# Kernel optimization log

Hardware: AMD Instinct MI355X
Metric: run time of the kernel (lower is better)

## Reference

```python
import jax, jax.numpy as jnp
import numpy as np

SP = 4      # sp_size (number of simulated sequence-parallel ranks)
NH = 16     # num_attention_heads
HD = 64     # head_dim
HS = 1024   # hidden_size
B = 1       # batch
S = 8192    # global sequence length (SP chunks of 2048)


def setup_inputs() -> dict:
    key = jax.random.key(0)
    ks = jax.random.split(key, 9)
    w_scale = 1.0 / np.sqrt(HS)
    def w(k):
        # xavier-ish init, stored as [in, out] so y = x @ W + b
        return jax.random.uniform(k, (HS, HS), jnp.float32, -w_scale, w_scale)
    return {
        'hidden_states': jax.random.normal(ks[0], (B, S, HS), jnp.float32),
        'Wq': w(ks[1]), 'bq': jnp.zeros((HS,), jnp.float32),
        'Wk': w(ks[2]), 'bk': jnp.zeros((HS,), jnp.float32),
        'Wv': w(ks[3]), 'bv': jnp.zeros((HS,), jnp.float32),
        'Wo': w(ks[4]), 'bo': jnp.zeros((HS,), jnp.float32),
    }


def reference(hidden_states, Wq, bq, Wk, bk, Wv, bv, Wo, bo):
    b, s, _ = hidden_states.shape
    sc = s // SP  # per-rank chunk length
    inv_sqrt_hd = 1.0 / np.sqrt(HD)

    def heads(x):
        # [B, S, HS] -> [SP, B, NH, Sc, HD]
        return x.reshape(b, SP, sc, NH, HD).transpose(1, 0, 3, 2, 4)

    q = heads(hidden_states @ Wq + bq)
    k = heads(hidden_states @ Wk + bk)
    v = heads(hidden_states @ Wv + bv)

    out = jnp.zeros_like(q)
    # ring attention: at step i each rank r attends to chunk (r + i) mod SP
    for i in range(SP):
        ki = jnp.roll(k, -i, axis=0)
        vi = jnp.roll(v, -i, axis=0)
        scores = jnp.einsum('sbhqd,sbhkd->sbhqk', q, ki) * inv_sqrt_hd
        probs = jax.nn.softmax(scores, axis=-1)  # per-chunk softmax (faithful to source)
        out = out + jnp.einsum('sbhqk,sbhkd->sbhqd', probs, vi)
    out = out / SP  # source divides accumulated context by sp_size

    # [SP, B, NH, Sc, HD] -> [B, S, NH*HD]
    ctx = out.transpose(1, 0, 3, 2, 4).reshape(b, s, NH * HD)
    return ctx @ Wo + bo
```

## Files before the change

kernel.cpp:

```cpp
#include <hip/hip_runtime.h>

#define DEVINL __device__ __forceinline__

typedef __attribute__((ext_vector_type(8))) short short8;
typedef __attribute__((ext_vector_type(4))) float floatx4;
typedef __attribute__((ext_vector_type(2))) unsigned uintx2;

DEVINL unsigned short f2bf(float f){
  unsigned u = __builtin_bit_cast(unsigned, f);
  u += 0x7FFFu + ((u >> 16) & 1u);
  return (unsigned short)(u >> 16);
}
DEVINL unsigned pk2(float a, float b){
  unsigned ua = __builtin_bit_cast(unsigned, a);
  unsigned ub = __builtin_bit_cast(unsigned, b);
  ua += 0x7FFFu + ((ua >> 16) & 1u);
  ub += 0x7FFFu + ((ub >> 16) & 1u);
  return (ua >> 16) | (ub & 0xFFFF0000u);
}
DEVINL unsigned pkfast(float a, float b){
  unsigned ua = __builtin_bit_cast(unsigned, a) + 0x8000u;
  unsigned ub = __builtin_bit_cast(unsigned, b) + 0x8000u;
  return __builtin_amdgcn_perm(ub, ua, 0x07060302u);
}
DEVINL float bf2f(unsigned short h){
  unsigned u = ((unsigned)h) << 16;
  return __builtin_bit_cast(float, u);
}
DEVINL void gload_lds16(const void* g, void* l){
  __builtin_amdgcn_global_load_lds((const __attribute__((address_space(1))) void*)g,
                                   (__attribute__((address_space(3))) void*)l, 16, 0, 0);
}
DEVINL int perm2(int k){
  return (((k >> 4) & 1) << 5) | (((k >> 2) & 3) << 3) | (((k >> 5) & 1) << 2) | (k & 3);
}

__global__ void k_detect(const unsigned* __restrict__ w, int* __restrict__ flag){
  __shared__ int cnt;
  if (threadIdx.x == 0) cnt = 0;
  __syncthreads();
  int c = 0;
  for (int i = threadIdx.x; i < 1024; i += 256){
    unsigned e = (w[i] >> 7) & 0xFFu;
    c += (e >= 120u && e <= 132u) ? 1 : 0;
  }
  atomicAdd(&cnt, c);
  __syncthreads();
  if (threadIdx.x == 0) *flag = (cnt > 512) ? 1 : 0;
}

__global__ void k_conv_bf16(const void* __restrict__ src, unsigned short* __restrict__ dst,
                            int n, const int* __restrict__ flag){
  int i = (blockIdx.x * 256 + threadIdx.x) * 8;
  if (i >= n) return;
  if (*flag){
    ((uint4*)dst)[i >> 3] = ((const uint4*)src)[i >> 3];
  } else {
    const float* s = (const float*)src;
    short8 v;
    #pragma unroll
    for (int j = 0; j < 8; j++) v[j] = (short)f2bf(s[i + j]);
    *(short8*)(dst + i) = v;
  }
}

__global__ void k_conv_wT4(const void* __restrict__ s0, const void* __restrict__ s1,
                           const void* __restrict__ s2, const void* __restrict__ s3,
                           unsigned short* __restrict__ d0, unsigned short* __restrict__ d1,
                           unsigned short* __restrict__ d2, unsigned short* __restrict__ d3,
                           const int* __restrict__ flag){
  __shared__ float tile[32][33];
  const void* src; unsigned short* dst;
  switch (blockIdx.z){
    case 0: src = s0; dst = d0; break;
    case 1: src = s1; dst = d1; break;
    case 2: src = s2; dst = d2; break;
    default: src = s3; dst = d3; break;
  }
  const int tx = threadIdx.x & 31, ty = threadIdx.x >> 5;
  const int bx = blockIdx.x, by = blockIdx.y;
  const int isbf = *flag;
  #pragma unroll
  for (int r = 0; r < 32; r += 8){
    int k = by*32 + ty + r, n = bx*32 + tx;
    float v = isbf ? bf2f(((const unsigned short*)src)[k*1024 + n])
                   : ((const float*)src)[k*1024 + n];
    tile[ty + r][tx] = v;
  }
  __syncthreads();
  #pragma unroll
  for (int r = 0; r < 32; r += 8){
    int n = bx*32 + ty + r, k = by*32 + tx;
    dst[n*1024 + k] = f2bf(tile[tx][ty + r]);
  }
}

__global__ void k_conv_b4(const void* __restrict__ s0, const void* __restrict__ s1,
                          const void* __restrict__ s2, const void* __restrict__ s3,
                          float* __restrict__ dst, const int* __restrict__ flag){
  int i = blockIdx.x * 256 + threadIdx.x;
  if (i >= 4096) return;
  int z = i >> 10, j = i & 1023;
  const void* s = (z == 0) ? s0 : (z == 1) ? s1 : (z == 2) ? s2 : s3;
  dst[i] = (*flag) ? bf2f(((const unsigned short*)s)[j]) : ((const float*)s)[j];
}

template<int MODE>
__global__ __launch_bounds__(256, 2) void k_gemm(
    const unsigned short* __restrict__ A, const unsigned short* __restrict__ Bt,
    const float* __restrict__ bias, void* __restrict__ C0, void* __restrict__ C1,
    void* __restrict__ C2, const int* __restrict__ flagp, float scale)
{
  const int K = 1024;
  __shared__ __align__(16) unsigned short As[128*32];
  __shared__ __align__(16) unsigned short Bs[128*32];
  const int tid = threadIdx.x;
  const int lane = tid & 63, wave = tid >> 6;
  const int quad = lane >> 4, l15 = lane & 15;
  const int m0 = blockIdx.x * 128, n0 = blockIdx.y * 128;
  const int wm = (wave >> 1) * 64, wn = (wave & 1) * 64;
  const floatx4 fzero = {0.f, 0.f, 0.f, 0.f};
  floatx4 acc[4][4];
  #pragma unroll
  for (int i = 0; i < 4; i++)
    #pragma unroll
    for (int j = 0; j < 4; j++) acc[i][j] = fzero;

  for (int k0 = 0; k0 < K; k0 += 32){
    __syncthreads();
    #pragma unroll
    for (int rep = 0; rep < 2; rep++){
      int idx = tid + rep*256;
      int row = idx >> 2, c = idx & 3;
      gload_lds16(A  + (size_t)(m0 + row)*K + (k0 + c*8), &As[idx*8]);
      gload_lds16(Bt + (size_t)(n0 + row)*K + (k0 + c*8), &Bs[idx*8]);
    }
    asm volatile("s_waitcnt vmcnt(0)" ::: "memory");
    __syncthreads();
    short8 af[4], bf[4];
    #pragma unroll
    for (int i = 0; i < 4; i++) af[i] = *(const short8*)&As[(wm + i*16 + l15)*32 + quad*8];
    #pragma unroll
    for (int j = 0; j < 4; j++) bf[j] = *(const short8*)&Bs[(wn + j*16 + l15)*32 + quad*8];
    #pragma unroll
    for (int i = 0; i < 4; i++)
      #pragma unroll
      for (int j = 0; j < 4; j++)
        acc[i][j] = __builtin_amdgcn_mfma_f32_16x16x32_bf16(af[i], bf[j], acc[i][j], 0, 0, 0);
  }

  float bs[4];
  #pragma unroll
  for (int j = 0; j < 4; j++) bs[j] = bias[n0 + wn + j*16 + l15];
  const int useBf = (MODE == 1) ? *flagp : 1;
  #pragma unroll
  for (int i = 0; i < 4; i++){
    #pragma unroll
    for (int j = 0; j < 4; j++){
      int n = n0 + wn + j*16 + l15;
      #pragma unroll
      for (int r = 0; r < 4; r++){
        int m = m0 + wm + i*16 + quad*4 + r;
        float v = acc[i][j][r] + bs[j];
        if (MODE == 3){
          int sel = n >> 10, nn = n & 1023;
          if (sel == 0){
            int dd = (nn & 63) ^ ((m & 7) << 3);
            ((unsigned short*)C0)[((size_t)(nn >> 6)*8192 + m)*64 + dd] = f2bf(v * scale);
          } else if (sel == 1){
            int dd = (nn & 63) ^ ((m & 7) << 3);
            ((unsigned short*)C1)[((size_t)(nn >> 6)*8192 + m)*64 + dd] = f2bf(v);
          } else {
            int s2 = perm2(m & 63) ^ ((nn & 7) << 3);
            ((unsigned short*)C2)[(size_t)nn*8192 + (m & ~63) + s2] = f2bf(v);
          }
        } else {
          if (useBf) ((unsigned short*)C0)[(size_t)m*1024 + n] = f2bf(v);
          else       ((float*)C0)[(size_t)m*1024 + n] = v;
        }
      }
    }
  }
}

__global__ __launch_bounds__(256, 2) void k_attn(
    const unsigned short* __restrict__ Qg, const unsigned short* __restrict__ Kg,
    const unsigned short* __restrict__ Vg, unsigned short* __restrict__ ctx)
{
  __shared__ __align__(16) unsigned short Qs[256*64];
  __shared__ __align__(16) unsigned short Ks[2][64*64];
  __shared__ __align__(16) unsigned short Vs[2][64*64];
  const int tid = threadIdx.x, lane = tid & 63, wave = tid >> 6;
  const int quad = lane >> 4, l15 = lane & 15;
  const int bid = blockIdx.x;
  const int xcd = bid & 7, slot = bid >> 3;
  const int h = xcd*2 + (slot >> 5);
  const int rem = slot & 31, rchunk = rem >> 3, qt = rem & 7;
  const int sq0 = rchunk*2048 + qt*256;
  const char* Qbase = (const char*)(Qg + (size_t)h*8192*64 + (size_t)sq0*64);
  const char* Kbase = (const char*)(Kg + (size_t)h*8192*64);
  const char* Vbase = (const char*)(Vg + (size_t)h*8192*64);
  const int wq0 = wave * 64;
  const floatx4 fzero = {0.f, 0.f, 0.f, 0.f};

  const int idx0 = tid, idx1 = tid + 256;
  const size_t voff0 = (size_t)(idx0 >> 3)*16384 + (idx0 & 7)*16;
  const size_t voff1 = (size_t)(idx1 >> 3)*16384 + (idx1 & 7)*16;

  auto stage = [&](int buf, int kvs){
    const char* Kt = Kbase + (size_t)kvs*128;
    const char* Vt = Vbase + (size_t)kvs*2;
    char* kd = (char*)Ks[buf];
    char* vd = (char*)Vs[buf];
    gload_lds16(Kt + idx0*16, kd + idx0*16);
    gload_lds16(Kt + idx1*16, kd + idx1*16);
    gload_lds16(Vt + voff0, vd + idx0*16);
    gload_lds16(Vt + voff1, vd + idx1*16);
  };

  #pragma unroll
  for (int rep = 0; rep < 8; rep++){
    int idx = tid + rep*256;
    gload_lds16(Qbase + idx*16, (char*)Qs + idx*16);
  }
  stage(0, rchunk*2048);
  asm volatile("s_waitcnt vmcnt(0)" ::: "memory");
  __syncthreads();

  short8 qf[4][2];
  #pragma unroll
  for (int mi = 0; mi < 4; mi++)
    #pragma unroll
    for (int ks = 0; ks < 2; ks++){
      int row = wq0 + mi*16 + l15;
      qf[mi][ks] = *(const short8*)&Qs[row*64 + (((ks*4 + quad) ^ (row & 7)))*8];
    }

  short8 ones;
  #pragma unroll
  for (int j = 0; j < 8; j++) ones[j] = (short)0x3F80;

  floatx4 Of[4][4];
  #pragma unroll
  for (int mi = 0; mi < 4; mi++)
    #pragma unroll
    for (int di = 0; di < 4; di++) Of[mi][di] = fzero;

  for (int i = 0; i < 4; i++){
    floatx4 Oc[4][4], Ol[4];
    #pragma unroll
    for (int mi = 0; mi < 4; mi++){
      Ol[mi] = fzero;
      #pragma unroll
      for (int di = 0; di < 4; di++) Oc[mi][di] = fzero;
    }

    for (int kt = 0; kt < 32; kt++){
      const int t = i*32 + kt, cur = t & 1;
      asm volatile("s_waitcnt vmcnt(0)" ::: "memory");
      __syncthreads();
      if (t < 127){
        int t1 = t + 1;
        int kvs = ((rchunk + (t1 >> 5)) & 3)*2048 + (t1 & 31)*64;
        stage(cur ^ 1, kvs);
      }

      short8 pf[4][2];
      #pragma unroll
      for (int mi = 0; mi < 4; mi++){
        floatx4 St[4];
        #pragma unroll
        for (int ni = 0; ni < 4; ni++) St[ni] = fzero;
        #pragma unroll
        for (int ks = 0; ks < 2; ks++)
          #pragma unroll
          for (int ni = 0; ni < 4; ni++){
            int krow = ni*16 + l15;
            short8 kf = *(const short8*)&Ks[cur][krow*64 + (((ks*4 + quad) ^ (krow & 7)))*8];
            St[ni] = __builtin_amdgcn_mfma_f32_16x16x32_bf16(kf, qf[mi][ks], St[ni], 0, 0, 0);
          }
        #pragma unroll
        for (int ni = 0; ni < 4; ni++)
          #pragma unroll
          for (int r = 0; r < 4; r++)
            St[ni][r] = __builtin_amdgcn_exp2f(St[ni][r]);
        #pragma unroll
        for (int ks = 0; ks < 2; ks++){
          uintx2 lo, hi;
          lo[0] = pkfast(St[ks  ][0], St[ks  ][1]);
          lo[1] = pkfast(St[ks  ][2], St[ks  ][3]);
          hi[0] = pkfast(St[2+ks][0], St[2+ks][1]);
          hi[1] = pkfast(St[2+ks][2], St[2+ks][3]);
          union { uintx2 u[2]; short8 s; } cv;
          cv.u[0] = lo; cv.u[1] = hi;
          pf[mi][ks] = cv.s;
        }
      }

      #pragma unroll
      for (int ks = 0; ks < 2; ks++){
        #pragma unroll
        for (int di = 0; di < 4; di++){
          int vrow = di*16 + l15;
          short8 vf = *(const short8*)&Vs[cur][vrow*64 + (((ks*4 + quad) ^ (vrow & 7)))*8];
          #pragma unroll
          for (int mi = 0; mi < 4; mi++)
            Oc[mi][di] = __builtin_amdgcn_mfma_f32_16x16x32_bf16(vf, pf[mi][ks], Oc[mi][di], 0, 0, 0);
        }
        #pragma unroll
        for (int mi = 0; mi < 4; mi++)
          Ol[mi] = __builtin_amdgcn_mfma_f32_16x16x32_bf16(ones, pf[mi][ks], Ol[mi], 0, 0, 0);
      }
    }

    #pragma unroll
    for (int mi = 0; mi < 4; mi++){
      float inv = __builtin_amdgcn_rcpf(Ol[mi][0]);
      #pragma unroll
      for (int di = 0; di < 4; di++)
        #pragma unroll
        for (int r = 0; r < 4; r++) Of[mi][di][r] += Oc[mi][di][r] * inv;
    }
  }

  #pragma unroll
  for (int mi = 0; mi < 4; mi++){
    int q = sq0 + wq0 + mi*16 + l15;
    #pragma unroll
    for (int di = 0; di < 4; di++){
      uintx2 w;
      w[0] = pk2(Of[mi][di][0]*0.25f, Of[mi][di][1]*0.25f);
      w[1] = pk2(Of[mi][di][2]*0.25f, Of[mi][di][3]*0.25f);
      *(uintx2*)&ctx[(size_t)q*1024 + h*64 + di*16 + quad*4] = w;
    }
  }
}

extern "C" void kernel_launch(void* const* d_in, const int* in_sizes, int n_in,
                              void* d_out, int out_size, void* d_ws, size_t ws_size,
                              hipStream_t stream)
{
  (void)in_sizes; (void)n_in; (void)out_size; (void)ws_size;
  char* ws = (char*)d_ws;
  size_t off = 0;
  auto alloc = [&](size_t bytes) -> char* {
    char* p = ws + off;
    off = (off + bytes + 255) & ~(size_t)255;
    return p;
  };
  int* flag            = (int*)alloc(4);
  unsigned short* hsb  = (unsigned short*)alloc((size_t)8192*1024*2);
  unsigned short* wqt  = (unsigned short*)alloc((size_t)1024*1024*2);
  unsigned short* wkt  = (unsigned short*)alloc((size_t)1024*1024*2);
  unsigned short* wvt  = (unsigned short*)alloc((size_t)1024*1024*2);
  unsigned short* wot  = (unsigned short*)alloc((size_t)1024*1024*2);
  float* biasAll       = (float*)alloc(4096*4);
  unsigned short* Qb   = (unsigned short*)alloc((size_t)16*8192*64*2);
  unsigned short* Kb   = (unsigned short*)alloc((size_t)16*8192*64*2);
  unsigned short* Vb   = (unsigned short*)alloc((size_t)16*8192*64*2);
  unsigned short* ctxb = (unsigned short*)alloc((size_t)8192*1024*2);

  k_detect<<<1, 256, 0, stream>>>((const unsigned*)d_in[0], flag);
  k_conv_bf16<<<4096, 256, 0, stream>>>(d_in[0], hsb, 8192*1024, flag);
  k_conv_wT4<<<dim3(32,32,4), 256, 0, stream>>>(d_in[1], d_in[3], d_in[5], d_in[7],
                                                wqt, wkt, wvt, wot, flag);
  k_conv_b4<<<16, 256, 0, stream>>>(d_in[2], d_in[4], d_in[6], d_in[8], biasAll, flag);

  const float Cs = 0.18033688011112042f;
  k_gemm<3><<<dim3(64, 24), 256, 0, stream>>>(hsb, wqt, biasAll, Qb, Kb, Vb, nullptr, Cs);

  k_attn<<<512, 256, 0, stream>>>(Qb, Kb, Vb, ctxb);

  k_gemm<1><<<dim3(64, 8), 256, 0, stream>>>(ctxb, wot, biasAll + 3072, d_out,
                                             nullptr, nullptr, flag, 1.0f);
}
```

Baseline: 483.1 us.

## Halve attention query tile to 128 rows, double grid, drop Q LDS staging

```diff
diff --git a/kernel.cpp b/kernel.cpp
--- a/kernel.cpp
+++ b/kernel.cpp
@@ -183,24 +183,23 @@
   }
 }
 
-__global__ __launch_bounds__(256, 2) void k_attn(
+__global__ __launch_bounds__(256, 4) void k_attn(
     const unsigned short* __restrict__ Qg, const unsigned short* __restrict__ Kg,
     const unsigned short* __restrict__ Vg, unsigned short* __restrict__ ctx)
 {
-  __shared__ __align__(16) unsigned short Qs[256*64];
   __shared__ __align__(16) unsigned short Ks[2][64*64];
   __shared__ __align__(16) unsigned short Vs[2][64*64];
   const int tid = threadIdx.x, lane = tid & 63, wave = tid >> 6;
   const int quad = lane >> 4, l15 = lane & 15;
   const int bid = blockIdx.x;
   const int xcd = bid & 7, slot = bid >> 3;
-  const int h = xcd*2 + (slot >> 5);
-  const int rem = slot & 31, rchunk = rem >> 3, qt = rem & 7;
-  const int sq0 = rchunk*2048 + qt*256;
-  const char* Qbase = (const char*)(Qg + (size_t)h*8192*64 + (size_t)sq0*64);
+  const int h = xcd*2 + (slot >> 6);
+  const int rem = slot & 63, rchunk = rem >> 4, qt = rem & 15;
+  const int sq0 = rchunk*2048 + qt*128;
+  const unsigned short* Qp = Qg + (size_t)h*8192*64 + (size_t)sq0*64;
   const char* Kbase = (const char*)(Kg + (size_t)h*8192*64);
   const char* Vbase = (const char*)(Vg + (size_t)h*8192*64);
-  const int wq0 = wave * 64;
+  const int wq0 = wave * 32;
   const floatx4 fzero = {0.f, 0.f, 0.f, 0.f};
 
   const int idx0 = tid, idx1 = tid + 256;
@@ -218,38 +217,33 @@
     gload_lds16(Vt + voff1, vd + idx1*16);
   };
 
-  #pragma unroll
-  for (int rep = 0; rep < 8; rep++){
-    int idx = tid + rep*256;
-    gload_lds16(Qbase + idx*16, (char*)Qs + idx*16);
-  }
+  short8 qf[2][2];
+  #pragma unroll
+  for (int mi = 0; mi < 2; mi++)
+    #pragma unroll
+    for (int ks = 0; ks < 2; ks++){
+      int row = wq0 + mi*16 + l15;
+      qf[mi][ks] = *(const short8*)&Qp[row*64 + (((ks*4 + quad) ^ (row & 7)))*8];
+    }
+
   stage(0, rchunk*2048);
   asm volatile("s_waitcnt vmcnt(0)" ::: "memory");
   __syncthreads();
 
-  short8 qf[4][2];
-  #pragma unroll
-  for (int mi = 0; mi < 4; mi++)
-    #pragma unroll
-    for (int ks = 0; ks < 2; ks++){
-      int row = wq0 + mi*16 + l15;
-      qf[mi][ks] = *(const short8*)&Qs[row*64 + (((ks*4 + quad) ^ (row & 7)))*8];
-    }
-
   short8 ones;
   #pragma unroll
   for (int j = 0; j < 8; j++) ones[j] = (short)0x3F80;
 
-  floatx4 Of[4][4];
-  #pragma unroll
-  for (int mi = 0; mi < 4; mi++)
+  floatx4 Of[2][4];
+  #pragma unroll
+  for (int mi = 0; mi < 2; mi++)
     #pragma unroll
     for (int di = 0; di < 4; di++) Of[mi][di] = fzero;
 
   for (int i = 0; i < 4; i++){
-    floatx4 Oc[4][4], Ol[4];
-    #pragma unroll
-    for (int mi = 0; mi < 4; mi++){
+    floatx4 Oc[2][4], Ol[2];
+    #pragma unroll
+    for (int mi = 0; mi < 2; mi++){
       Ol[mi] = fzero;
       #pragma unroll
       for (int di = 0; di < 4; di++) Oc[mi][di] = fzero;
@@ -265,35 +259,38 @@
         stage(cur ^ 1, kvs);
       }
 
-      short8 pf[4][2];
-      #pragma unroll
-      for (int mi = 0; mi < 4; mi++){
-        floatx4 St[4];
-        #pragma unroll
-        for (int ni = 0; ni < 4; ni++) St[ni] = fzero;
-        #pragma unroll
-        for (int ks = 0; ks < 2; ks++)
+      short8 pf[2][2];
+      #pragma unroll
+      for (int g = 0; g < 2; g++){
+        floatx4 Sa[2], Sb[2];
+        #pragma unroll
+        for (int mi = 0; mi < 2; mi++){ Sa[mi] = fzero; Sb[mi] = fzero; }
+        #pragma unroll
+        for (int ks = 0; ks < 2; ks++){
+          int krowA = g*16 + l15, krowB = (g + 2)*16 + l15;
+          short8 kfa = *(const short8*)&Ks[cur][krowA*64 + (((ks*4 + quad) ^ (krowA & 7)))*8];
+          short8 kfb = *(const short8*)&Ks[cur][krowB*64 + (((ks*4 + quad) ^ (krowB & 7)))*8];
           #pragma unroll
-          for (int ni = 0; ni < 4; ni++){
-            int krow = ni*16 + l15;
-            short8 kf = *(const short8*)&Ks[cur][krow*64 + (((ks*4 + quad) ^ (krow & 7)))*8];
-            St[ni] = __builtin_amdgcn_mfma_f32_16x16x32_bf16(kf, qf[mi][ks], St[ni], 0, 0, 0);
+          for (int mi = 0; mi < 2; mi++){
+            Sa[mi] = __builtin_amdgcn_mfma_f32_16x16x32_bf16(kfa, qf[mi][ks], Sa[mi], 0, 0, 0);
+            Sb[mi] = __builtin_amdgcn_mfma_f32_16x16x32_bf16(kfb, qf[mi][ks], Sb[mi], 0, 0, 0);
           }
-        #pragma unroll
-        for (int ni = 0; ni < 4; ni++)
+        }
+        #pragma unroll
+        for (int mi = 0; mi < 2; mi++){
           #pragma unroll
-          for (int r = 0; r < 4; r++)
-            St[ni][r] = __builtin_amdgcn_exp2f(St[ni][r]);
-        #pragma unroll
-        for (int ks = 0; ks < 2; ks++){
+          for (int r = 0; r < 4; r++){
+            Sa[mi][r] = __builtin_amdgcn_exp2f(Sa[mi][r]);
+            Sb[mi][r] = __builtin_amdgcn_exp2f(Sb[mi][r]);
+          }
           uintx2 lo, hi;
-          lo[0] = pkfast(St[ks  ][0], St[ks  ][1]);
-          lo[1] = pkfast(St[ks  ][2], St[ks  ][3]);
-          hi[0] = pkfast(St[2+ks][0], St[2+ks][1]);
-          hi[1] = pkfast(St[2+ks][2], St[2+ks][3]);
+          lo[0] = pkfast(Sa[mi][0], Sa[mi][1]);
+          lo[1] = pkfast(Sa[mi][2], Sa[mi][3]);
+          hi[0] = pkfast(Sb[mi][0], Sb[mi][1]);
+          hi[1] = pkfast(Sb[mi][2], Sb[mi][3]);
           union { uintx2 u[2]; short8 s; } cv;
           cv.u[0] = lo; cv.u[1] = hi;
-          pf[mi][ks] = cv.s;
+          pf[mi][g] = cv.s;
         }
       }
 
@@ -303,18 +300,16 @@
         for (int di = 0; di < 4; di++){
           int vrow = di*16 + l15;
           short8 vf = *(const short8*)&Vs[cur][vrow*64 + (((ks*4 + quad) ^ (vrow & 7)))*8];
-          #pragma unroll
-          for (int mi = 0; mi < 4; mi++)
-            Oc[mi][di] = __builtin_amdgcn_mfma_f32_16x16x32_bf16(vf, pf[mi][ks], Oc[mi][di], 0, 0, 0);
+          Oc[0][di] = __builtin_amdgcn_mfma_f32_16x16x32_bf16(vf, pf[0][ks], Oc[0][di], 0, 0, 0);
+          Oc[1][di] = __builtin_amdgcn_mfma_f32_16x16x32_bf16(vf, pf[1][ks], Oc[1][di], 0, 0, 0);
         }
-        #pragma unroll
-        for (int mi = 0; mi < 4; mi++)
-          Ol[mi] = __builtin_amdgcn_mfma_f32_16x16x32_bf16(ones, pf[mi][ks], Ol[mi], 0, 0, 0);
+        Ol[0] = __builtin_amdgcn_mfma_f32_16x16x32_bf16(ones, pf[0][ks], Ol[0], 0, 0, 0);
+        Ol[1] = __builtin_amdgcn_mfma_f32_16x16x32_bf16(ones, pf[1][ks], Ol[1], 0, 0, 0);
       }
     }
 
     #pragma unroll
-    for (int mi = 0; mi < 4; mi++){
+    for (int mi = 0; mi < 2; mi++){
       float inv = __builtin_amdgcn_rcpf(Ol[mi][0]);
       #pragma unroll
       for (int di = 0; di < 4; di++)
@@ -324,7 +319,7 @@
   }
 
   #pragma unroll
-  for (int mi = 0; mi < 4; mi++){
+  for (int mi = 0; mi < 2; mi++){
     int q = sq0 + wq0 + mi*16 + l15;
     #pragma unroll
     for (int di = 0; di < 4; di++){
@@ -369,7 +364,7 @@
   const float Cs = 0.18033688011112042f;
   k_gemm<3><<<dim3(64, 24), 256, 0, stream>>>(hsb, wqt, biasAll, Qb, Kb, Vb, nullptr, Cs);
 
-  k_attn<<<512, 256, 0, stream>>>(Qb, Kb, Vb, ctxb);
+  k_attn<<<1024, 256, 0, stream>>>(Qb, Kb, Vb, ctxb);
 
   k_gemm<1><<<dim3(64, 8), 256, 0, stream>>>(ctxb, wot, biasAll + 3072, d_out,
                                              nullptr, nullptr, flag, 1.0f);
```

New measurement: 507.8 us. 1.05x slower.

## Restructure attention inner loop: VALU row sums, reload Q from LDS, unroll buffers

Applied to the files above, without the earlier changes.

```diff
diff --git a/kernel.cpp b/kernel.cpp
--- a/kernel.cpp
+++ b/kernel.cpp
@@ -188,8 +188,7 @@
     const unsigned short* __restrict__ Vg, unsigned short* __restrict__ ctx)
 {
   __shared__ __align__(16) unsigned short Qs[256*64];
-  __shared__ __align__(16) unsigned short Ks[2][64*64];
-  __shared__ __align__(16) unsigned short Vs[2][64*64];
+  __shared__ __align__(16) unsigned short KV[2*64*64*2];
   const int tid = threadIdx.x, lane = tid & 63, wave = tid >> 6;
   const int quad = lane >> 4, l15 = lane & 15;
   const int bid = blockIdx.x;
@@ -210,8 +209,8 @@
   auto stage = [&](int buf, int kvs){
     const char* Kt = Kbase + (size_t)kvs*128;
     const char* Vt = Vbase + (size_t)kvs*2;
-    char* kd = (char*)Ks[buf];
-    char* vd = (char*)Vs[buf];
+    char* kd = (char*)KV + buf*8192;
+    char* vd = (char*)KV + 16384 + buf*8192;
     gload_lds16(Kt + idx0*16, kd + idx0*16);
     gload_lds16(Kt + idx1*16, kd + idx1*16);
     gload_lds16(Vt + voff0, vd + idx0*16);
@@ -224,104 +223,109 @@
     gload_lds16(Qbase + idx*16, (char*)Qs + idx*16);
   }
   stage(0, rchunk*2048);
+
+  const int swz0 = ((0*4 + quad) ^ (l15 & 7)) * 16;
+  const int swz1 = ((1*4 + quad) ^ (l15 & 7)) * 16;
+  const char* kvb0 = (const char*)KV + l15*128 + swz0;
+  const char* kvb1 = (const char*)KV + l15*128 + swz1;
+  const char* qb0  = (const char*)Qs + (wq0 + l15)*128 + swz0;
+  const char* qb1  = (const char*)Qs + (wq0 + l15)*128 + swz1;
+
   asm volatile("s_waitcnt vmcnt(0)" ::: "memory");
   __syncthreads();
 
-  short8 qf[4][2];
+  floatx4 Of[4][4];
   #pragma unroll
   for (int mi = 0; mi < 4; mi++)
     #pragma unroll
-    for (int ks = 0; ks < 2; ks++){
-      int row = wq0 + mi*16 + l15;
-      qf[mi][ks] = *(const short8*)&Qs[row*64 + (((ks*4 + quad) ^ (row & 7)))*8];
-    }
-
-  short8 ones;
-  #pragma unroll
-  for (int j = 0; j < 8; j++) ones[j] = (short)0x3F80;
-
-  floatx4 Of[4][4];
-  #pragma unroll
-  for (int mi = 0; mi < 4; mi++)
-    #pragma unroll
     for (int di = 0; di < 4; di++) Of[mi][di] = fzero;
 
+#define TILE_BODY(CUR, TT)                                                          \
+  {                                                                                 \
+    asm volatile("s_waitcnt vmcnt(0)" ::: "memory");            \
+    __syncthreads();                                         \
+    if ((TT) < 127){                                                                \
+      int t1 = (TT) + 1;                                                            \
+      int kvs = ((rchunk + (t1 >> 5)) & 3)*2048 + (t1 & 31)*64;                     \
+      stage((CUR) ^ 1, kvs);                           \
+    }                                                                               \
+    short8 vf[2][4];                                                                \
+    _Pragma("unroll")                                                               \
+    for (int di = 0; di < 4; di++){                                                 \
+      vf[0][di] = *(const short8*)(kvb0 + (16384 + (CUR)*8192) + di*2048);          \
+      vf[1][di] = *(const short8*)(kvb1 + (16384 + (CUR)*8192) + di*2048);          \
+    }                                                                               \
+    _Pragma("unroll")                                                               \
+    for (int mi = 0; mi < 4; mi++){                                                 \
+      short8 q0 = *(const short8*)(qb0 + mi*2048);                                  \
+      short8 q1 = *(const short8*)(qb1 + mi*2048);                                  \
+      floatx4 St[4];                                                                \
+      _Pragma("unroll")                                                             \
+      for (int ni = 0; ni < 4; ni++) St[ni] = fzero;                                \
+      _Pragma("unroll")                                                             \
+      for (int ni = 0; ni < 4; ni++){                                               \
+        short8 kf0 = *(const short8*)(kvb0 + (CUR)*8192 + ni*2048);                 \
+        short8 kf1 = *(const short8*)(kvb1 + (CUR)*8192 + ni*2048);                 \
+        St[ni] = __builtin_amdgcn_mfma_f32_16x16x32_bf16(kf0, q0, St[ni], 0, 0, 0); \
+        St[ni] = __builtin_amdgcn_mfma_f32_16x16x32_bf16(kf1, q1, St[ni], 0, 0, 0); \
+      }                                                                             \
+      _Pragma("unroll")                                                             \
+      for (int ni = 0; ni < 4; ni++)                                                \
+        _Pragma("unroll")                                                           \
+        for (int r = 0; r < 4; r++)                                                 \
+          St[ni][r] = __builtin_amdgcn_exp2f(St[ni][r]);                            \
+      {                                                                             \
+        float t0 = (St[0][0] + St[0][1]) + (St[0][2] + St[0][3]);                   \
+        float t1 = (St[1][0] + St[1][1]) + (St[1][2] + St[1][3]);                   \
+        float t2 = (St[2][0] + St[2][1]) + (St[2][2] + St[2][3]);                   \
+        float t3 = (St[3][0] + St[3][1]) + (St[3][2] + St[3][3]);                   \
+        Olp[mi] += (t0 + t2) + (t1 + t3);                                           \
+      }                                                                             \
+      short8 pf0, pf1;                                                              \
+      {                                                                             \
+        uintx2 lo, hi;                                                              \
+        union { uintx2 u[2]; short8 s; } cv;                                        \
+        lo[0] = pkfast(St[0][0], St[0][1]); lo[1] = pkfast(St[0][2], St[0][3]);     \
+        hi[0] = pkfast(St[2][0], St[2][1]); hi[1] = pkfast(St[2][2], St[2][3]);     \
+        cv.u[0] = lo; cv.u[1] = hi; pf0 = cv.s;                                     \
+        lo[0] = pkfast(St[1][0], St[1][1]); lo[1] = pkfast(St[1][2], St[1][3]);     \
+        hi[0] = pkfast(St[3][0], St[3][1]); hi[1] = pkfast(St[3][2], St[3][3]);     \
+        cv.u[0] = lo; cv.u[1] = hi; pf1 = cv.s;                                     \
+      }                                                                             \
+      _Pragma("unroll")                                                             \
+      for (int di = 0; di < 4; di++){                                               \
+        Oc[mi][di] = __builtin_amdgcn_mfma_f32_16x16x32_bf16(vf[0][di], pf0, Oc[mi][di], 0, 0, 0); \
+        Oc[mi][di] = __builtin_amdgcn_mfma_f32_16x16x32_bf16(vf[1][di], pf1, Oc[mi][di], 0, 0, 0); \
+      }                                                                             \
+    }                                                                               \
+  }
+
   for (int i = 0; i < 4; i++){
-    floatx4 Oc[4][4], Ol[4];
-    #pragma unroll
-    for (int mi = 0; mi < 4; mi++){
-      Ol[mi] = fzero;
+    floatx4 Oc[4][4];
+    float Olp[4] = {0.f, 0.f, 0.f, 0.f};
+    #pragma unroll
+    for (int mi = 0; mi < 4; mi++)
       #pragma unroll
       for (int di = 0; di < 4; di++) Oc[mi][di] = fzero;
-    }
-
-    for (int kt = 0; kt < 32; kt++){
-      const int t = i*32 + kt, cur = t & 1;
-      asm volatile("s_waitcnt vmcnt(0)" ::: "memory");
-      __syncthreads();
-      if (t < 127){
-        int t1 = t + 1;
-        int kvs = ((rchunk + (t1 >> 5)) & 3)*2048 + (t1 & 31)*64;
-        stage(cur ^ 1, kvs);
-      }
-
-      short8 pf[4][2];
-      #pragma unroll
-      for (int mi = 0; mi < 4; mi++){
-        floatx4 St[4];
-        #pragma unroll
-        for (int ni = 0; ni < 4; ni++) St[ni] = fzero;
-        #pragma unroll
-        for (int ks = 0; ks < 2; ks++)
-          #pragma unroll
-          for (int ni = 0; ni < 4; ni++){
-            int krow = ni*16 + l15;
-            short8 kf = *(const short8*)&Ks[cur][krow*64 + (((ks*4 + quad) ^ (krow & 7)))*8];
-            St[ni] = __builtin_amdgcn_mfma_f32_16x16x32_bf16(kf, qf[mi][ks], St[ni], 0, 0, 0);
-          }
-        #pragma unroll
-        for (int ni = 0; ni < 4; ni++)
-          #pragma unroll
-          for (int r = 0; r < 4; r++)
-            St[ni][r] = __builtin_amdgcn_exp2f(St[ni][r]);
-        #pragma unroll
-        for (int ks = 0; ks < 2; ks++){
-          uintx2 lo, hi;
-          lo[0] = pkfast(St[ks  ][0], St[ks  ][1]);
-          lo[1] = pkfast(St[ks  ][2], St[ks  ][3]);
-          hi[0] = pkfast(St[2+ks][0], St[2+ks][1]);
-          hi[1] = pkfast(St[2+ks][2], St[2+ks][3]);
-          union { uintx2 u[2]; short8 s; } cv;
-          cv.u[0] = lo; cv.u[1] = hi;
-          pf[mi][ks] = cv.s;
-        }
-      }
-
-      #pragma unroll
-      for (int ks = 0; ks < 2; ks++){
-        #pragma unroll
-        for (int di = 0; di < 4; di++){
-          int vrow = di*16 + l15;
-          short8 vf = *(const short8*)&Vs[cur][vrow*64 + (((ks*4 + quad) ^ (vrow & 7)))*8];
-          #pragma unroll
-          for (int mi = 0; mi < 4; mi++)
-            Oc[mi][di] = __builtin_amdgcn_mfma_f32_16x16x32_bf16(vf, pf[mi][ks], Oc[mi][di], 0, 0, 0);
-        }
-        #pragma unroll
-        for (int mi = 0; mi < 4; mi++)
-          Ol[mi] = __builtin_amdgcn_mfma_f32_16x16x32_bf16(ones, pf[mi][ks], Ol[mi], 0, 0, 0);
-      }
+
+    for (int kt = 0; kt < 32; kt += 2){
+      TILE_BODY(0, i*32 + kt)
+      TILE_BODY(1, i*32 + kt + 1)
     }
 
     #pragma unroll
     for (int mi = 0; mi < 4; mi++){
-      float inv = __builtin_amdgcn_rcpf(Ol[mi][0]);
+      float l = Olp[mi];
+      l += __shfl_xor(l, 16);
+      l += __shfl_xor(l, 32);
+      float inv = __builtin_amdgcn_rcpf(l);
       #pragma unroll
       for (int di = 0; di < 4; di++)
         #pragma unroll
         for (int r = 0; r < 4; r++) Of[mi][di][r] += Oc[mi][di][r] * inv;
     }
   }
+#undef TILE_BODY
 
   #pragma unroll
   for (int mi = 0; mi < 4; mi++){
```

After: 500.0 us. +3.5%, slower.

## Split attention across ring chunks into parallel blocks with fp32 partial reduction

Applied to the files above, without the earlier changes.

```diff
diff --git a/kernel.cpp b/kernel.cpp
--- a/kernel.cpp
+++ b/kernel.cpp
@@ -183,6 +183,156 @@
   }
 }
 
+__global__ __launch_bounds__(256, 3) void k_attn2(
+    const unsigned short* __restrict__ Qg, const unsigned short* __restrict__ Kg,
+    const unsigned short* __restrict__ Vg, float* __restrict__ part)
+{
+  __shared__ __align__(16) unsigned short Ks[2][64*64];
+  __shared__ __align__(16) unsigned short Vs[2][64*64];
+  const int tid = threadIdx.x, lane = tid & 63, wave = tid >> 6;
+  const int quad = lane >> 4, l15 = lane & 15;
+  const int bid = blockIdx.x;
+  const int xcd = bid & 7, slot = bid >> 3;
+  const int h = xcd*2 + (slot >> 8);
+  const int rem = slot & 255;
+  const int c = rem >> 6, qt = rem & 63;
+  const int sq0 = qt*128;
+  const unsigned short* Qp = Qg + (size_t)h*8192*64 + (size_t)sq0*64;
+  const char* Kbase = (const char*)(Kg + (size_t)h*8192*64);
+  const char* Vbase = (const char*)(Vg + (size_t)h*8192*64);
+  const int wq0 = wave * 32;
+  const floatx4 fzero = {0.f, 0.f, 0.f, 0.f};
+
+  const int idx0 = tid, idx1 = tid + 256;
+  const size_t voff0 = (size_t)(idx0 >> 3)*16384 + (idx0 & 7)*16;
+  const size_t voff1 = (size_t)(idx1 >> 3)*16384 + (idx1 & 7)*16;
+
+  auto stage = [&](int buf, int kvs){
+    const char* Kt = Kbase + (size_t)kvs*128;
+    const char* Vt = Vbase + (size_t)kvs*2;
+    char* kd = (char*)Ks[buf];
+    char* vd = (char*)Vs[buf];
+    gload_lds16(Kt + idx0*16, kd + idx0*16);
+    gload_lds16(Kt + idx1*16, kd + idx1*16);
+    gload_lds16(Vt + voff0, vd + idx0*16);
+    gload_lds16(Vt + voff1, vd + idx1*16);
+  };
+
+  short8 qf[2][2];
+  #pragma unroll
+  for (int mi = 0; mi < 2; mi++)
+    #pragma unroll
+    for (int ks = 0; ks < 2; ks++){
+      int row = wq0 + mi*16 + l15;
+      qf[mi][ks] = *(const short8*)&Qp[row*64 + (((ks*4 + quad) ^ (row & 7)))*8];
+    }
+
+  stage(0, c*2048);
+  asm volatile("s_waitcnt vmcnt(0)" ::: "memory");
+  __syncthreads();
+
+  short8 ones;
+  #pragma unroll
+  for (int j = 0; j < 8; j++) ones[j] = (short)0x3F80;
+
+  floatx4 Oc[2][4], Ol[2];
+  #pragma unroll
+  for (int mi = 0; mi < 2; mi++){
+    Ol[mi] = fzero;
+    #pragma unroll
+    for (int di = 0; di < 4; di++) Oc[mi][di] = fzero;
+  }
+
+  for (int kt = 0; kt < 32; kt++){
+    const int cur = kt & 1;
+    asm volatile("s_waitcnt vmcnt(0)" ::: "memory");
+    __syncthreads();
+    if (kt < 31)
+      stage(cur ^ 1, c*2048 + (kt + 1)*64);
+
+    short8 pf[2][2];
+    {
+      floatx4 S0[4], S1[4];
+      #pragma unroll
+      for (int ni = 0; ni < 4; ni++){ S0[ni] = fzero; S1[ni] = fzero; }
+      #pragma unroll
+      for (int ks = 0; ks < 2; ks++)
+        #pragma unroll
+        for (int ni = 0; ni < 4; ni++){
+          int krow = ni*16 + l15;
+          short8 kf = *(const short8*)&Ks[cur][krow*64 + (((ks*4 + quad) ^ (krow & 7)))*8];
+          S0[ni] = __builtin_amdgcn_mfma_f32_16x16x32_bf16(kf, qf[0][ks], S0[ni], 0, 0, 0);
+          S1[ni] = __builtin_amdgcn_mfma_f32_16x16x32_bf16(kf, qf[1][ks], S1[ni], 0, 0, 0);
+        }
+      #pragma unroll
+      for (int ni = 0; ni < 4; ni++)
+        #pragma unroll
+        for (int r = 0; r < 4; r++){
+          S0[ni][r] = __builtin_amdgcn_exp2f(S0[ni][r]);
+          S1[ni][r] = __builtin_amdgcn_exp2f(S1[ni][r]);
+        }
+      #pragma unroll
+      for (int ks = 0; ks < 2; ks++){
+        uintx2 lo, hi;
+        union { uintx2 u[2]; short8 s; } cv;
+        lo[0] = pkfast(S0[ks  ][0], S0[ks  ][1]);
+        lo[1] = pkfast(S0[ks  ][2], S0[ks  ][3]);
+        hi[0] = pkfast(S0[2+ks][0], S0[2+ks][1]);
+        hi[1] = pkfast(S0[2+ks][2], S0[2+ks][3]);
+        cv.u[0] = lo; cv.u[1] = hi;
+        pf[0][ks] = cv.s;
+        lo[0] = pkfast(S1[ks  ][0], S1[ks  ][1]);
+        lo[1] = pkfast(S1[ks  ][2], S1[ks  ][3]);
+        hi[0] = pkfast(S1[2+ks][0], S1[2+ks][1]);
+        hi[1] = pkfast(S1[2+ks][2], S1[2+ks][3]);
+        cv.u[0] = lo; cv.u[1] = hi;
+        pf[1][ks] = cv.s;
+      }
+    }
+
+    #pragma unroll
+    for (int ks = 0; ks < 2; ks++){
+      #pragma unroll
+      for (int di = 0; di < 4; di++){
+        int vrow = di*16 + l15;
+        short8 vf = *(const short8*)&Vs[cur][vrow*64 + (((ks*4 + quad) ^ (vrow & 7)))*8];
+        Oc[0][di] = __builtin_amdgcn_mfma_f32_16x16x32_bf16(vf, pf[0][ks], Oc[0][di], 0, 0, 0);
+        Oc[1][di] = __builtin_amdgcn_mfma_f32_16x16x32_bf16(vf, pf[1][ks], Oc[1][di], 0, 0, 0);
+      }
+      Ol[0] = __builtin_amdgcn_mfma_f32_16x16x32_bf16(ones, pf[0][ks], Ol[0], 0, 0, 0);
+      Ol[1] = __builtin_amdgcn_mfma_f32_16x16x32_bf16(ones, pf[1][ks], Ol[1], 0, 0, 0);
+    }
+  }
+
+  #pragma unroll
+  for (int mi = 0; mi < 2; mi++){
+    float inv = __builtin_amdgcn_rcpf(Ol[mi][0]);
+    int q = sq0 + wq0 + mi*16 + l15;
+    float* dst = part + ((size_t)c*8192 + q)*1024 + h*64;
+    #pragma unroll
+    for (int di = 0; di < 4; di++){
+      floatx4 w;
+      #pragma unroll
+      for (int r = 0; r < 4; r++) w[r] = Oc[mi][di][r] * inv;
+      *(floatx4*)(dst + di*16 + quad*4) = w;
+    }
+  }
+}
+
+__global__ void k_reduce(const float* __restrict__ part, unsigned short* __restrict__ ctx){
+  const size_t N = (size_t)8192*1024;
+  size_t i = ((size_t)blockIdx.x*256 + threadIdx.x)*4;
+  if (i >= N) return;
+  floatx4 a = *(const floatx4*)(part + i);
+  floatx4 b = *(const floatx4*)(part + N + i);
+  floatx4 c = *(const floatx4*)(part + 2*N + i);
+  floatx4 d = *(const floatx4*)(part + 3*N + i);
+  uintx2 w;
+  w[0] = pk2(((a[0]+b[0])+(c[0]+d[0]))*0.25f, ((a[1]+b[1])+(c[1]+d[1]))*0.25f);
+  w[1] = pk2(((a[2]+b[2])+(c[2]+d[2]))*0.25f, ((a[3]+b[3])+(c[3]+d[3]))*0.25f);
+  *(uintx2*)&ctx[i] = w;
+}
+
 __global__ __launch_bounds__(256, 2) void k_attn(
     const unsigned short* __restrict__ Qg, const unsigned short* __restrict__ Kg,
     const unsigned short* __restrict__ Vg, unsigned short* __restrict__ ctx)
@@ -340,7 +490,7 @@
                               void* d_out, int out_size, void* d_ws, size_t ws_size,
                               hipStream_t stream)
 {
-  (void)in_sizes; (void)n_in; (void)out_size; (void)ws_size;
+  (void)in_sizes; (void)n_in; (void)out_size;
   char* ws = (char*)d_ws;
   size_t off = 0;
   auto alloc = [&](size_t bytes) -> char* {
@@ -359,6 +509,8 @@
   unsigned short* Kb   = (unsigned short*)alloc((size_t)16*8192*64*2);
   unsigned short* Vb   = (unsigned short*)alloc((size_t)16*8192*64*2);
   unsigned short* ctxb = (unsigned short*)alloc((size_t)8192*1024*2);
+  float* part          = (float*)alloc((size_t)4*8192*1024*4);
+  const bool wide = (off <= ws_size);
 
   k_detect<<<1, 256, 0, stream>>>((const unsigned*)d_in[0], flag);
   k_conv_bf16<<<4096, 256, 0, stream>>>(d_in[0], hsb, 8192*1024, flag);
@@ -369,7 +521,12 @@
   const float Cs = 0.18033688011112042f;
   k_gemm<3><<<dim3(64, 24), 256, 0, stream>>>(hsb, wqt, biasAll, Qb, Kb, Vb, nullptr, Cs);
 
-  k_attn<<<512, 256, 0, stream>>>(Qb, Kb, Vb, ctxb);
+  if (wide){
+    k_attn2<<<4096, 256, 0, stream>>>(Qb, Kb, Vb, part);
+    k_reduce<<<8192, 256, 0, stream>>>(part, ctxb);
+  } else {
+    k_attn<<<512, 256, 0, stream>>>(Qb, Kb, Vb, ctxb);
+  }
 
   k_gemm<1><<<dim3(64, 8), 256, 0, stream>>>(ctxb, wot, biasAll + 3072, d_out,
                                              nullptr, nullptr, flag, 1.0f);
```

After: 499.3 us. +3.4%, slower.
